# Kernel optimization log

Measured on AMD Instinct MI355X. Metric: run time of the kernel, lower is better.

Reference implementation:

```python
import jax, jax.numpy as jnp
import numpy as np

D_MODEL = 512

def setup_inputs() -> dict:
    key = jax.random.key(0)
    k1, k2, k3, k4, k5 = jax.random.split(key, 5)
    x = jax.random.normal(k1, (8, D_MODEL, 2048), dtype=jnp.float32)
    s = 1.0 / np.sqrt(D_MODEL)
    W_qkv = jax.random.uniform(k2, (D_MODEL, 3 * D_MODEL), dtype=jnp.float32, minval=-s, maxval=s)
    b_qkv = jax.random.uniform(k3, (3 * D_MODEL,), dtype=jnp.float32, minval=-s, maxval=s)
    W_proj = jax.random.uniform(k4, (D_MODEL, D_MODEL), dtype=jnp.float32, minval=-s, maxval=s)
    b_proj = jax.random.uniform(k5, (D_MODEL,), dtype=jnp.float32, minval=-s, maxval=s)
    return {"x": x, "W_qkv": W_qkv, "b_qkv": b_qkv, "W_proj": W_proj, "b_proj": b_proj}

def reference(x, W_qkv, b_qkv, W_proj, b_proj):
    # x: [B, L, N] with L == d_model; attend across the N variable axis
    xt = jnp.swapaxes(x, 1, 2)                      # [B, N, L]
    L = xt.shape[-1]
    qkv = xt @ W_qkv + b_qkv                        # [B, N, 3L]
    q, k, v = jnp.split(qkv, 3, axis=-1)            # each [B, N, L]
    attn = jnp.einsum('bnd,bmd->bnm', q, k) / jnp.sqrt(jnp.float32(L))
    attn = jax.nn.softmax(attn, axis=-1)            # [B, N, N]
    out = jnp.einsum('bnm,bmd->bnd', attn, v)       # [B, N, L]
    out = out @ W_proj + b_proj                     # [B, N, L]
    return jnp.swapaxes(out, 1, 2)                  # [B, L, N]
```

## Files before the change

### kernel.cpp

```cpp
#include <hip/hip_runtime.h>

#define NVAR 2048
#define DM   512
#define J3   1536

typedef _Float16 f16;
typedef _Float16 f16x8 __attribute__((ext_vector_type(8)));
typedef _Float16 f16x4 __attribute__((ext_vector_type(4)));
typedef float    f32x4 __attribute__((ext_vector_type(4)));

#define SBAR() do { asm volatile("s_barrier" ::: "memory"); \
                    __builtin_amdgcn_sched_barrier(0); } while(0)
#define LGKM0() do { asm volatile("s_waitcnt lgkmcnt(0)" ::: "memory"); \
                     __builtin_amdgcn_sched_barrier(0); } while(0)
#define GLOAD(gp, lp) __builtin_amdgcn_global_load_lds( \
    (const __attribute__((address_space(1))) void*)(gp), \
    (__attribute__((address_space(3))) void*)(lp), 16, 0, 0)

__device__ __forceinline__ void waitvm_n(int n) {
    switch (n) {
    case 0: asm volatile("s_waitcnt vmcnt(0)" ::: "memory"); break;
    case 1: asm volatile("s_waitcnt vmcnt(1)" ::: "memory"); break;
    case 2: asm volatile("s_waitcnt vmcnt(2)" ::: "memory"); break;
    case 3: asm volatile("s_waitcnt vmcnt(3)" ::: "memory"); break;
    case 4: asm volatile("s_waitcnt vmcnt(4)" ::: "memory"); break;
    case 5: asm volatile("s_waitcnt vmcnt(5)" ::: "memory"); break;
    case 6: asm volatile("s_waitcnt vmcnt(6)" ::: "memory"); break;
    case 7: asm volatile("s_waitcnt vmcnt(7)" ::: "memory"); break;
    case 8: asm volatile("s_waitcnt vmcnt(8)" ::: "memory"); break;
    default: break;
    }
    __builtin_amdgcn_sched_barrier(0);
}

__global__ __launch_bounds__(256)
void k_tr(const float* __restrict__ src, f16* __restrict__ dst,
          int R, int C, long bsSrc, long bsDst) {
    __shared__ float t[64][65];
    const float* s = src + (size_t)blockIdx.z * bsSrc;
    f16* d = dst + (size_t)blockIdx.z * bsDst;
    const int c0 = blockIdx.x * 64, r0 = blockIdx.y * 64;
    const int lx = threadIdx.x & 15, ly = threadIdx.x >> 4;
#pragma unroll
    for (int p = 0; p < 4; ++p) {
        int r = p * 16 + ly;
        f32x4 v = *(const f32x4*)(s + (size_t)(r0 + r) * C + c0 + lx * 4);
#pragma unroll
        for (int i = 0; i < 4; ++i) t[r][lx * 4 + i] = v[i];
    }
    __syncthreads();
#pragma unroll
    for (int p = 0; p < 4; ++p) {
        int c = p * 16 + ly;
        f16x4 h;
#pragma unroll
        for (int i = 0; i < 4; ++i) h[i] = (f16)t[lx * 4 + i][c];
        *(f16x4*)(d + (size_t)(c0 + c) * R + r0 + lx * 4) = h;
    }
}

__global__ __launch_bounds__(256)
void k_cast(const float* __restrict__ W, f16* __restrict__ out) {
    int idx = blockIdx.x * 256 + threadIdx.x;
    int gi = idx * 4;
    int d = gi >> 9, j = gi & 511;
    f32x4 v = *(const f32x4*)(W + (size_t)d * J3 + 1024 + j);
    f16x4 h;
#pragma unroll
    for (int i = 0; i < 4; ++i) h[i] = (f16)v[i];
    *(f16x4*)(out + (size_t)d * 512 + j) = h;
}

__global__ __launch_bounds__(256)
void k_bvp(const float* __restrict__ bqkv, const float* __restrict__ Wp,
           float* __restrict__ bias_c) {
    const int b = blockIdx.x;
    const int lt = threadIdx.x & 63, js = threadIdx.x >> 6;
    const int l = b * 64 + lt;
    float s = 0.f;
    for (int j = js * 128; j < js * 128 + 128; ++j)
        s += bqkv[1024 + j] * Wp[(size_t)j * DM + l];
    __shared__ float red[4][64];
    red[js][lt] = s;
    __syncthreads();
    if (js == 0)
        bias_c[1024 + l] = (red[0][lt] + red[1][lt]) + (red[2][lt] + red[3][lt]);
    if (threadIdx.x < 128) {
        int i = b * 128 + threadIdx.x;
        bias_c[i] = bqkv[i];
    }
}

#define ASZ (256 * 64)
__global__ __launch_bounds__(512, 2)
void gemm_sp(const f16* __restrict__ A, const f16* __restrict__ B,
             long bsA, long bsB, int lda, int ldb, int K,
             float scale, f16* __restrict__ o0) {
    __shared__ f16 smem[5 * ASZ];
    f16* sA = smem;
    f16* sB = smem + 3 * ASZ;

    const int tid  = threadIdx.x;
    const int lane = tid & 63;
    const int w    = __builtin_amdgcn_readfirstlane(tid >> 6);
    const int wm   = (w >> 2) * 128;
    const int wn   = (w & 3) * 64;
    const int z    = blockIdx.x;
    const int bid  = blockIdx.y;
    const int bxA  = bid & 7;
    const int bxB  = bid >> 3;

    const f16* Ab = A + (size_t)z * bsA + (size_t)bxA * 256 * lda;
    const f16* Bb = B + (size_t)z * bsB + (size_t)bxB * 256 * ldb;

    int offA[2][2], offB[2][2];
#pragma unroll
    for (int h = 0; h < 2; ++h)
#pragma unroll
        for (int i = 0; i < 2; ++i) {
            int slot = i * 512 + tid;
            int row  = h * 128 + (slot >> 3);
            int s    = (slot & 7) ^ (row & 7);
            offA[h][i] = row * lda + s * 8;
            offB[h][i] = row * ldb + s * 8;
        }

    auto STG_A = [&](int kt, int h, int buf) {
        f16* d = sA + buf * ASZ + h * 8192;
#pragma unroll
        for (int i = 0; i < 2; ++i)
            GLOAD(Ab + offA[h][i] + kt * 64, d + (i * 512 + tid) * 8);
    };
    auto STG_B = [&](int kt, int h, int buf) {
        f16* d = sB + buf * ASZ + h * 8192;
#pragma unroll
        for (int i = 0; i < 2; ++i)
            GLOAD(Bb + offB[h][i] + kt * 64, d + (i * 512 + tid) * 8);
    };

    int koff[2];
#pragma unroll
    for (int ks = 0; ks < 2; ++ks)
        koff[ks] = ((ks * 4 + (lane >> 4)) ^ (lane & 7)) * 8;
    const int rowA = (wm + (lane & 15)) * 64;
    const int rowB = (wn + (lane & 15)) * 64;

    f16x8 av[8][2], bv[4][2];
    f32x4 acc[8][4] = {};

    auto LD_AV = [&](const f16* p, int mi0) {
#pragma unroll
        for (int mi = 0; mi < 4; ++mi)
#pragma unroll
            for (int ks = 0; ks < 2; ++ks)
                av[mi0 + mi][ks] = *(const f16x8*)(p + rowA + (mi0 + mi) * 1024 + koff[ks]);
    };
    auto LD_BV = [&](const f16* p, int nj0) {
#pragma unroll
        for (int nj = 0; nj < 2; ++nj)
#pragma unroll
            for (int ks = 0; ks < 2; ++ks)
                bv[nj0 + nj][ks] = *(const f16x8*)(p + rowB + (nj0 + nj) * 1024 + koff[ks]);
    };
    auto MM = [&](int mi0, int nj0) {
        __builtin_amdgcn_s_setprio(1);
#pragma unroll
        for (int mi = 0; mi < 4; ++mi)
#pragma unroll
            for (int nj = 0; nj < 2; ++nj)
#pragma unroll
                for (int ks = 0; ks < 2; ++ks)
                    acc[mi0 + mi][nj0 + nj] = __builtin_amdgcn_mfma_f32_16x16x32_f16(
                        av[mi0 + mi][ks], bv[nj0 + nj][ks], acc[mi0 + mi][nj0 + nj], 0, 0, 0);
        __builtin_amdgcn_s_setprio(0);
    };

    const int NT = K >> 6;
    int issued = 0, markB = 0;

    STG_A(0, 0, 0); STG_A(0, 1, 0); issued += 4;
    STG_B(0, 0, 0); STG_B(0, 1, 0); issued += 4; markB = issued;
    if (NT > 1) { STG_A(1, 0, 1); STG_A(1, 1, 1); issued += 4; }
    waitvm_n(issued - markB);
    SBAR();

    int iA = 0, iB = 0;
    for (int t = 0; t < NT; ++t) {
        const f16* pA = sA + iA * ASZ;
        const f16* pB = sB + iB * ASZ;
        const int bufB2 = iB ^ 1;
        int bufA2 = iA + 2; if (bufA2 >= 3) bufA2 -= 3;

        LD_BV(pB, 0); LD_AV(pA, 0);
        if (t + 1 < NT) { STG_B(t + 1, 0, bufB2); issued += 2; }
        SBAR(); LGKM0();
        MM(0, 0);
        SBAR();

        LD_BV(pB, 2);
        if (t + 1 < NT) { STG_B(t + 1, 1, bufB2); issued += 2; markB = issued; }
        SBAR(); LGKM0();
        MM(0, 2);
        SBAR();

        LD_AV(pA, 4);
        if (t + 2 < NT) { STG_A(t + 2, 0, bufA2); issued += 2; }
        SBAR(); LGKM0();
        MM(4, 2);
        SBAR();

        if (t + 2 < NT) { STG_A(t + 2, 1, bufA2); issued += 2; }
        if (t + 1 < NT) { waitvm_n(issued - markB); SBAR(); }
        MM(4, 0);
        if (t + 1 < NT) SBAR();

        iA = (iA + 1 == 3) ? 0 : iA + 1;
        iB ^= 1;
    }

    const int n0 = bxB * 256;
    const int m0 = bxA * 256;
    f16* bb = smem;
#pragma unroll
    for (int mi = 0; mi < 8; ++mi) {
        const int m    = wm + mi * 16 + ((lane >> 4) << 2);
        const int c16  = m >> 3;
        const int half = m & 4;
#pragma unroll
        for (int nj = 0; nj < 4; ++nj) {
            const int nl = wn + nj * 16 + (lane & 15);
            f16x4 vv;
#pragma unroll
            for (int r = 0; r < 4; ++r)
                vv[r] = (f16)__expf(acc[mi][nj][r] * scale);
            *(f16x4*)(bb + nl * 256 + ((c16 ^ (nl & 7)) << 3) + half) = vv;
        }
    }
    LGKM0();
    SBAR();
#pragma unroll
    for (int it = 0; it < 16; ++it) {
        const int row = it * 16 + (tid >> 5);
        const int ch  = tid & 31;
        f16x8 v = *(const f16x8*)(bb + row * 256 + ((ch ^ (row & 7)) << 3));
        *(f16x8*)(o0 + ((size_t)z * NVAR + n0 + row) * NVAR + m0 + ch * 8) = v;
    }
}

#define AO (128 * 64)
#define BO (256 * 64)
__global__ __launch_bounds__(512, 2)
void gemm_out(const f16* __restrict__ A, const f16* __restrict__ B,
              long bsA, long bsB, int lda, int ldb, int K,
              const float* __restrict__ bias, float* __restrict__ of) {
    __shared__ f16 smem[3 * AO + 2 * BO];
    f16* sA = smem;
    f16* sB = smem + 3 * AO;

    const int tid  = threadIdx.x;
    const int lane = tid & 63;
    const int w    = __builtin_amdgcn_readfirstlane(tid >> 6);
    const int wm   = (w >> 2) * 64;
    const int wn   = (w & 3) * 64;
    const int z    = blockIdx.x;
    const int bid  = blockIdx.y;
    const int bxA  = bid & 15;
    const int bxB  = bid >> 4;

    const f16* Ab = A + (size_t)z * bsA + (size_t)bxA * 128 * lda;
    const f16* Bb = B + (size_t)z * bsB + (size_t)bxB * 256 * ldb;

    int offA[2], offB[4];
#pragma unroll
    for (int i = 0; i < 2; ++i) {
        int slot = i * 512 + tid;
        int row  = slot >> 3;
        int s    = (slot & 7) ^ (row & 7);
        offA[i] = row * lda + s * 8;
    }
#pragma unroll
    for (int i = 0; i < 4; ++i) {
        int slot = i * 512 + tid;
        int row  = slot >> 3;
        int s    = (slot & 7) ^ (row & 7);
        offB[i] = row * ldb + s * 8;
    }

    auto STG_A = [&](int kt, int buf) {
        f16* d = sA + buf * AO;
#pragma unroll
        for (int i = 0; i < 2; ++i)
            GLOAD(Ab + offA[i] + kt * 64, d + (i * 512 + tid) * 8);
    };
    auto STG_B = [&](int kt, int buf) {
        f16* d = sB + buf * BO;
#pragma unroll
        for (int i = 0; i < 4; ++i)
            GLOAD(Bb + offB[i] + kt * 64, d + (i * 512 + tid) * 8);
    };

    int koff[2];
#pragma unroll
    for (int ks = 0; ks < 2; ++ks)
        koff[ks] = ((ks * 4 + (lane >> 4)) ^ (lane & 7)) * 8;
    const int rowA = (wm + (lane & 15)) * 64;
    const int rowB = (wn + (lane & 15)) * 64;

    f16x8 ones;
#pragma unroll
    for (int e = 0; e < 8; ++e) ones[e] = (f16)1.0f;

    f16x8 av[4][2], bv[4][2];
    f32x4 acc[4][4] = {};
    f32x4 accrs[4] = {};

    auto LD_AV = [&](const f16* p, int mi0) {
#pragma unroll
        for (int mi = 0; mi < 2; ++mi)
#pragma unroll
            for (int ks = 0; ks < 2; ++ks)
                av[mi0 + mi][ks] = *(const f16x8*)(p + rowA + (mi0 + mi) * 1024 + koff[ks]);
    };
    auto LD_BV = [&](const f16* p) {
#pragma unroll
        for (int nj = 0; nj < 4; ++nj)
#pragma unroll
            for (int ks = 0; ks < 2; ++ks)
                bv[nj][ks] = *(const f16x8*)(p + rowB + nj * 1024 + koff[ks]);
    };
    auto MM = [&](int mi0) {
        __builtin_amdgcn_s_setprio(1);
#pragma unroll
        for (int mi = 0; mi < 2; ++mi)
#pragma unroll
            for (int ks = 0; ks < 2; ++ks) {
                accrs[mi0 + mi] = __builtin_amdgcn_mfma_f32_16x16x32_f16(
                    av[mi0 + mi][ks], ones, accrs[mi0 + mi], 0, 0, 0);
#pragma unroll
                for (int nj = 0; nj < 4; ++nj)
                    acc[mi0 + mi][nj] = __builtin_amdgcn_mfma_f32_16x16x32_f16(
                        av[mi0 + mi][ks], bv[nj][ks], acc[mi0 + mi][nj], 0, 0, 0);
            }
        __builtin_amdgcn_s_setprio(0);
    };

    const int NT = K >> 6;
    int issued = 0, markB = 0;

    STG_A(0, 0); issued += 2;
    STG_B(0, 0); issued += 4; markB = issued;
    if (NT > 1) { STG_A(1, 1); issued += 2; }
    waitvm_n(issued - markB);
    SBAR();

    int iA = 0, iB = 0;
    for (int t = 0; t < NT; ++t) {
        const f16* pA = sA + iA * AO;
        const f16* pB = sB + iB * BO;
        int bufA2 = iA + 2; if (bufA2 >= 3) bufA2 -= 3;

        LD_BV(pB); LD_AV(pA, 0);
        if (t + 1 < NT) { STG_B(t + 1, iB ^ 1); issued += 4; markB = issued; }
        SBAR(); LGKM0();
        MM(0);
        SBAR();

        LD_AV(pA, 2);
        if (t + 2 < NT) { STG_A(t + 2, bufA2); issued += 2; }
        SBAR(); LGKM0();
        MM(2);
        if (t + 1 < NT) { waitvm_n(issued - markB); SBAR(); }

        iA = (iA + 1 == 3) ? 0 : iA + 1;
        iB ^= 1;
    }

    const int rb0 = bxA * 128 + wm + (lane >> 4) * 4;
    const int cb0 = bxB * 256 + wn + (lane & 15);
#pragma unroll
    for (int mi = 0; mi < 4; ++mi) {
        f32x4 inv;
#pragma unroll
        for (int r = 0; r < 4; ++r) inv[r] = 1.0f / accrs[mi][r];
#pragma unroll
        for (int nj = 0; nj < 4; ++nj) {
            const int l = cb0 + nj * 16;
            const float bb = bias[l];
            f32x4 vv;
#pragma unroll
            for (int r = 0; r < 4; ++r) vv[r] = acc[mi][nj][r] * inv[r] + bb;
            *(f32x4*)(of + ((size_t)z * DM + l) * NVAR + rb0 + mi * 16) = vv;
        }
    }
}

template<int MODE>
__global__ __launch_bounds__(256)
void gemm_f16(const f16* __restrict__ A, const f16* __restrict__ B,
              long bsA, long bsB, int lda, int ldb, int K, int nbx,
              const float* __restrict__ bias,
              f16* __restrict__ o0, f16* __restrict__ o1, f16* __restrict__ o2) {
    __shared__ f16 sA[128 * 64];
    __shared__ f16 sB[128 * 64];
    const int tid  = threadIdx.x;
    const int lane = tid & 63;
    const int w    = __builtin_amdgcn_readfirstlane(tid >> 6);
    const int wm   = (w >> 1) * 64;
    const int wn   = (w & 1) * 64;
    const int z    = blockIdx.x;
    const int bid  = blockIdx.y;
    const int bxA  = bid % nbx;
    const int bxB  = bid / nbx;

    const f16* Ab = A + (size_t)z * bsA + (size_t)bxA * 128 * lda;
    const f16* Bb = B + (size_t)z * bsB + (size_t)bxB * 128 * ldb;

    int srcA[4], srcB[4];
#pragma unroll
    for (int i = 0; i < 4; ++i) {
        int slot = i * 256 + tid;
        int row  = slot >> 3;
        int s    = (slot & 7) ^ (row & 7);
        srcA[i] = row * lda + s * 8;
        srcB[i] = row * ldb + s * 8;
    }

    f32x4 acc[4][4] = {};

    for (int k0 = 0; k0 < K; k0 += 64) {
        __syncthreads();
#pragma unroll
        for (int i = 0; i < 4; ++i) {
            GLOAD(Ab + srcA[i] + k0, sA + i * 2048 + w * 512);
            GLOAD(Bb + srcB[i] + k0, sB + i * 2048 + w * 512);
        }
        __syncthreads();
#pragma unroll
        for (int kh = 0; kh < 2; ++kh) {
            f16x8 av[4], bv[4];
#pragma unroll
            for (int mi = 0; mi < 4; ++mi) {
                int r = wm + mi * 16 + (lane & 15);
                int s = (kh * 4 + (lane >> 4)) ^ (r & 7);
                av[mi] = *(const f16x8*)(sA + r * 64 + s * 8);
            }
#pragma unroll
            for (int nj = 0; nj < 4; ++nj) {
                int r = wn + nj * 16 + (lane & 15);
                int s = (kh * 4 + (lane >> 4)) ^ (r & 7);
                bv[nj] = *(const f16x8*)(sB + r * 64 + s * 8);
            }
#pragma unroll
            for (int mi = 0; mi < 4; ++mi)
#pragma unroll
                for (int nj = 0; nj < 4; ++nj)
                    acc[mi][nj] = __builtin_amdgcn_mfma_f32_16x16x32_f16(
                        av[mi], bv[nj], acc[mi][nj], 0, 0, 0);
        }
    }

    const int rb0 = bxA * 128 + wm + (lane >> 4) * 4;
    const int cb0 = bxB * 128 + wn + (lane & 15);

    if (MODE == 0) {
        const int seg = (bxA * 128) >> 9;
#pragma unroll
        for (int mi = 0; mi < 4; ++mi) {
            const int j = rb0 + mi * 16;
            const f32x4 b4 = *(const f32x4*)(bias + j);
#pragma unroll
            for (int nj = 0; nj < 4; ++nj) {
                const int n = cb0 + nj * 16;
                if (seg == 2) {
#pragma unroll
                    for (int r = 0; r < 4; ++r)
                        o2[((size_t)z * DM + (j - 1024 + r)) * NVAR + n] =
                            (f16)(acc[mi][nj][r] + b4[r]);
                } else {
                    f16* dst = seg ? o1 : o0;
                    const int jj = seg ? j - 512 : j;
                    f16x4 vv;
#pragma unroll
                    for (int r = 0; r < 4; ++r) vv[r] = (f16)(acc[mi][nj][r] + b4[r]);
                    *(f16x4*)(dst + ((size_t)z * NVAR + n) * DM + jj) = vv;
                }
            }
        }
    } else {
#pragma unroll
        for (int mi = 0; mi < 4; ++mi)
#pragma unroll
            for (int nj = 0; nj < 4; ++nj) {
                f16x4 vv;
#pragma unroll
                for (int r = 0; r < 4; ++r) vv[r] = (f16)acc[mi][nj][r];
                *(f16x4*)(o0 + ((size_t)(cb0 + nj * 16)) * DM
                               + rb0 + mi * 16) = vv;
            }
    }
}

extern "C" void kernel_launch(void* const* d_in, const int* in_sizes, int n_in,
                              void* d_out, int out_size, void* d_ws, size_t ws_size,
                              hipStream_t stream) {
    const float* x     = (const float*)d_in[0];
    const float* Wqkv  = (const float*)d_in[1];
    const float* bqkv  = (const float*)d_in[2];
    const float* Wproj = (const float*)d_in[3];
    const float* bproj = (const float*)d_in[4];
    float* out = (float*)d_out;

    const size_t PB = (size_t)NVAR * DM;
    f16* xT   = (f16*)d_ws;
    f16* q    = xT + 8 * PB;
    f16* kk   = q  + 8 * PB;
    f16* vwT  = kk + 8 * PB;
    f16* S    = vwT + 8 * PB;
    f16* scr  = S  + (size_t)8 * NVAR * NVAR;
    f16* WqT  = scr + 8 * PB;
    f16* WpT  = WqT + (size_t)J3 * DM;
    f16* Wq2  = scr;
    float* bias_c = (float*)(scr + 512 * 512);

    k_tr<<<dim3(NVAR / 64, DM / 64, 8), 256, 0, stream>>>(
        x, xT, DM, NVAR, (long)DM * NVAR, (long)NVAR * DM);
    k_tr<<<dim3(16, DM / 64, 1), 256, 0, stream>>>(Wqkv, WqT, DM, J3, 0, 0);
    k_tr<<<dim3(DM / 64, DM / 64, 1), 256, 0, stream>>>(Wproj, WpT, DM, DM, 0, 0);
    k_cast<<<dim3(256), 256, 0, stream>>>(Wqkv, Wq2);
    k_bvp<<<dim3(8), 256, 0, stream>>>(bqkv, Wproj, bias_c);

    gemm_f16<4><<<dim3(1, 16), 256, 0, stream>>>(
        Wq2, WpT, 0, 0, 512, DM, DM, 4,
        nullptr, WqT + (size_t)1024 * DM, nullptr, nullptr);

    gemm_f16<0><<<dim3(8, 12 * 16), 256, 0, stream>>>(
        WqT, xT, 0, (long)NVAR * DM, DM, DM, DM, 12,
        bias_c, q, kk, vwT);

    gemm_sp<<<dim3(8, 8 * 8), 512, 0, stream>>>(
        kk, q, (long)NVAR * DM, (long)NVAR * DM, DM, DM, DM,
        0.044194173824159216f, S);

    gemm_out<<<dim3(8, 32), 512, 0, stream>>>(
        S, vwT, (long)NVAR * NVAR, (long)DM * NVAR, NVAR, NVAR, NVAR,
        bproj, out);
}
```

Measured before the change: 173.6 us.

## Split QKV projection into large-tile QK GEMM and separate V GEMM

```diff
diff --git a/kernel.cpp b/kernel.cpp
--- a/kernel.cpp
+++ b/kernel.cpp
@@ -60,42 +60,69 @@
 }
 
 __global__ __launch_bounds__(256)
-void k_cast(const float* __restrict__ W, f16* __restrict__ out) {
-    int idx = blockIdx.x * 256 + threadIdx.x;
-    int gi = idx * 4;
-    int d = gi >> 9, j = gi & 511;
-    f32x4 v = *(const f32x4*)(W + (size_t)d * J3 + 1024 + j);
-    f16x4 h;
-#pragma unroll
-    for (int i = 0; i < 4; ++i) h[i] = (f16)v[i];
-    *(f16x4*)(out + (size_t)d * 512 + j) = h;
-}
-
-__global__ __launch_bounds__(256)
-void k_bvp(const float* __restrict__ bqkv, const float* __restrict__ Wp,
-           float* __restrict__ bias_c) {
+void k_prep(const float* __restrict__ Wqkv, const float* __restrict__ Wproj,
+            const float* __restrict__ bqkv,
+            f16* __restrict__ WqT, f16* __restrict__ WpT,
+            f16* __restrict__ Wq2, float* __restrict__ bias_c) {
+    __shared__ float t[64][65];
     const int b = blockIdx.x;
-    const int lt = threadIdx.x & 63, js = threadIdx.x >> 6;
-    const int l = b * 64 + lt;
-    float s = 0.f;
-    for (int j = js * 128; j < js * 128 + 128; ++j)
-        s += bqkv[1024 + j] * Wp[(size_t)j * DM + l];
-    __shared__ float red[4][64];
-    red[js][lt] = s;
-    __syncthreads();
-    if (js == 0)
-        bias_c[1024 + l] = (red[0][lt] + red[1][lt]) + (red[2][lt] + red[3][lt]);
-    if (threadIdx.x < 128) {
-        int i = b * 128 + threadIdx.x;
-        bias_c[i] = bqkv[i];
+    if (b < 192) {
+        const float* s; f16* d; int R, C, bx, by;
+        if (b < 128) { s = Wqkv; d = WqT; R = DM; C = J3; bx = b & 15; by = b >> 4; }
+        else { s = Wproj; d = WpT; R = DM; C = DM; bx = (b - 128) & 7; by = (b - 128) >> 3; }
+        const int c0 = bx * 64, r0 = by * 64;
+        const int lx = threadIdx.x & 15, ly = threadIdx.x >> 4;
+#pragma unroll
+        for (int p = 0; p < 4; ++p) {
+            int r = p * 16 + ly;
+            f32x4 v = *(const f32x4*)(s + (size_t)(r0 + r) * C + c0 + lx * 4);
+#pragma unroll
+            for (int i = 0; i < 4; ++i) t[r][lx * 4 + i] = v[i];
+        }
+        __syncthreads();
+#pragma unroll
+        for (int p = 0; p < 4; ++p) {
+            int c = p * 16 + ly;
+            f16x4 h;
+#pragma unroll
+            for (int i = 0; i < 4; ++i) h[i] = (f16)t[lx * 4 + i][c];
+            *(f16x4*)(d + (size_t)(c0 + c) * R + r0 + lx * 4) = h;
+        }
+    } else if (b < 448) {
+        int idx = (b - 192) * 256 + threadIdx.x;
+        int gi = idx * 4;
+        int d = gi >> 9, j = gi & 511;
+        f32x4 v = *(const f32x4*)(Wqkv + (size_t)d * J3 + 1024 + j);
+        f16x4 h;
+#pragma unroll
+        for (int i = 0; i < 4; ++i) h[i] = (f16)v[i];
+        *(f16x4*)(Wq2 + (size_t)d * 512 + j) = h;
+    } else {
+        const int bb = b - 448;
+        const int lt = threadIdx.x & 63, js = threadIdx.x >> 6;
+        const int l = bb * 64 + lt;
+        float s = 0.f;
+        for (int j = js * 128; j < js * 128 + 128; ++j)
+            s += bqkv[1024 + j] * Wproj[(size_t)j * DM + l];
+        float* red = &t[0][0];
+        red[js * 64 + lt] = s;
+        __syncthreads();
+        if (js == 0)
+            bias_c[1024 + l] = (red[lt] + red[64 + lt]) + (red[128 + lt] + red[192 + lt]);
+        if (threadIdx.x < 128) {
+            int i = bb * 128 + threadIdx.x;
+            bias_c[i] = bqkv[i];
+        }
     }
 }
 
 #define ASZ (256 * 64)
+template<int MODE, int ABITS>
 __global__ __launch_bounds__(512, 2)
 void gemm_sp(const f16* __restrict__ A, const f16* __restrict__ B,
              long bsA, long bsB, int lda, int ldb, int K,
-             float scale, f16* __restrict__ o0) {
+             const float* __restrict__ bias, float scale,
+             f16* __restrict__ o0, f16* __restrict__ o1) {
     __shared__ f16 smem[5 * ASZ];
     f16* sA = smem;
     f16* sB = smem + 3 * ASZ;
@@ -107,8 +134,8 @@
     const int wn   = (w & 3) * 64;
     const int z    = blockIdx.x;
     const int bid  = blockIdx.y;
-    const int bxA  = bid & 7;
-    const int bxB  = bid >> 3;
+    const int bxA  = bid & ((1 << ABITS) - 1);
+    const int bxB  = bid >> ABITS;
 
     const f16* Ab = A + (size_t)z * bsA + (size_t)bxA * 256 * lda;
     const f16* Bb = B + (size_t)z * bsB + (size_t)bxB * 256 * ldb;
@@ -218,32 +245,53 @@
         iB ^= 1;
     }
 
-    const int n0 = bxB * 256;
-    const int m0 = bxA * 256;
-    f16* bb = smem;
-#pragma unroll
-    for (int mi = 0; mi < 8; ++mi) {
-        const int m    = wm + mi * 16 + ((lane >> 4) << 2);
-        const int c16  = m >> 3;
-        const int half = m & 4;
-#pragma unroll
-        for (int nj = 0; nj < 4; ++nj) {
-            const int nl = wn + nj * 16 + (lane & 15);
-            f16x4 vv;
-#pragma unroll
-            for (int r = 0; r < 4; ++r)
-                vv[r] = (f16)__expf(acc[mi][nj][r] * scale);
-            *(f16x4*)(bb + nl * 256 + ((c16 ^ (nl & 7)) << 3) + half) = vv;
-        }
-    }
-    LGKM0();
-    SBAR();
-#pragma unroll
-    for (int it = 0; it < 16; ++it) {
-        const int row = it * 16 + (tid >> 5);
-        const int ch  = tid & 31;
-        f16x8 v = *(const f16x8*)(bb + row * 256 + ((ch ^ (row & 7)) << 3));
-        *(f16x8*)(o0 + ((size_t)z * NVAR + n0 + row) * NVAR + m0 + ch * 8) = v;
+    if (MODE == 0) {
+        const int seg = bxA >> 1;
+        f16* dst = seg ? o1 : o0;
+        const int rb0 = bxA * 256 + wm + (lane >> 4) * 4;
+        const int cb0 = bxB * 256 + wn + (lane & 15);
+#pragma unroll
+        for (int mi = 0; mi < 8; ++mi) {
+            const int j = rb0 + mi * 16;
+            const int jj = j - seg * 512;
+            const f32x4 b4 = *(const f32x4*)(bias + j);
+#pragma unroll
+            for (int nj = 0; nj < 4; ++nj) {
+                const int n = cb0 + nj * 16;
+                f16x4 vv;
+#pragma unroll
+                for (int r = 0; r < 4; ++r) vv[r] = (f16)(acc[mi][nj][r] + b4[r]);
+                *(f16x4*)(dst + ((size_t)z * NVAR + n) * DM + jj) = vv;
+            }
+        }
+    } else {
+        const int n0 = bxB * 256;
+        const int m0 = bxA * 256;
+        f16* bb = smem;
+#pragma unroll
+        for (int mi = 0; mi < 8; ++mi) {
+            const int m    = wm + mi * 16 + ((lane >> 4) << 2);
+            const int c16  = m >> 3;
+            const int half = m & 4;
+#pragma unroll
+            for (int nj = 0; nj < 4; ++nj) {
+                const int nl = wn + nj * 16 + (lane & 15);
+                f16x4 vv;
+#pragma unroll
+                for (int r = 0; r < 4; ++r)
+                    vv[r] = (f16)__expf(acc[mi][nj][r] * scale);
+                *(f16x4*)(bb + nl * 256 + ((c16 ^ (nl & 7)) << 3) + half) = vv;
+            }
+        }
+        LGKM0();
+        SBAR();
+#pragma unroll
+        for (int it = 0; it < 16; ++it) {
+            const int row = it * 16 + (tid >> 5);
+            const int ch  = tid & 31;
+            f16x8 v = *(const f16x8*)(bb + row * 256 + ((ch ^ (row & 7)) << 3));
+            *(f16x8*)(o0 + ((size_t)z * NVAR + n0 + row) * NVAR + m0 + ch * 8) = v;
+        }
     }
 }
 
@@ -398,8 +446,7 @@
 __global__ __launch_bounds__(256)
 void gemm_f16(const f16* __restrict__ A, const f16* __restrict__ B,
               long bsA, long bsB, int lda, int ldb, int K, int nbx,
-              const float* __restrict__ bias,
-              f16* __restrict__ o0, f16* __restrict__ o1, f16* __restrict__ o2) {
+              const float* __restrict__ bias, f16* __restrict__ o0) {
     __shared__ f16 sA[128 * 64];
     __shared__ f16 sB[128 * 64];
     const int tid  = threadIdx.x;
@@ -462,31 +509,7 @@
     const int rb0 = bxA * 128 + wm + (lane >> 4) * 4;
     const int cb0 = bxB * 128 + wn + (lane & 15);
 
-    if (MODE == 0) {
-        const int seg = (bxA * 128) >> 9;
-#pragma unroll
-        for (int mi = 0; mi < 4; ++mi) {
-            const int j = rb0 + mi * 16;
-            const f32x4 b4 = *(const f32x4*)(bias + j);
-#pragma unroll
-            for (int nj = 0; nj < 4; ++nj) {
-                const int n = cb0 + nj * 16;
-                if (seg == 2) {
-#pragma unroll
-                    for (int r = 0; r < 4; ++r)
-                        o2[((size_t)z * DM + (j - 1024 + r)) * NVAR + n] =
-                            (f16)(acc[mi][nj][r] + b4[r]);
-                } else {
-                    f16* dst = seg ? o1 : o0;
-                    const int jj = seg ? j - 512 : j;
-                    f16x4 vv;
-#pragma unroll
-                    for (int r = 0; r < 4; ++r) vv[r] = (f16)(acc[mi][nj][r] + b4[r]);
-                    *(f16x4*)(dst + ((size_t)z * NVAR + n) * DM + jj) = vv;
-                }
-            }
-        }
-    } else {
+    if (MODE == 4) {
 #pragma unroll
         for (int mi = 0; mi < 4; ++mi)
 #pragma unroll
@@ -496,6 +519,18 @@
                 for (int r = 0; r < 4; ++r) vv[r] = (f16)acc[mi][nj][r];
                 *(f16x4*)(o0 + ((size_t)(cb0 + nj * 16)) * DM
                                + rb0 + mi * 16) = vv;
+            }
+    } else {
+#pragma unroll
+        for (int mi = 0; mi < 4; ++mi)
+#pragma unroll
+            for (int nj = 0; nj < 4; ++nj) {
+                const int l = cb0 + nj * 16;
+                const float bb = bias[l];
+                f16x4 vv;
+#pragma unroll
+                for (int r = 0; r < 4; ++r) vv[r] = (f16)(acc[mi][nj][r] + bb);
+                *(f16x4*)(o0 + ((size_t)z * DM + l) * NVAR + rb0 + mi * 16) = vv;
             }
     }
 }
@@ -518,28 +553,29 @@
     f16* S    = vwT + 8 * PB;
     f16* scr  = S  + (size_t)8 * NVAR * NVAR;
     f16* WqT  = scr + 8 * PB;
+    f16* WvpT = WqT + (size_t)1024 * DM;
     f16* WpT  = WqT + (size_t)J3 * DM;
     f16* Wq2  = scr;
     float* bias_c = (float*)(scr + 512 * 512);
 
     k_tr<<<dim3(NVAR / 64, DM / 64, 8), 256, 0, stream>>>(
         x, xT, DM, NVAR, (long)DM * NVAR, (long)NVAR * DM);
-    k_tr<<<dim3(16, DM / 64, 1), 256, 0, stream>>>(Wqkv, WqT, DM, J3, 0, 0);
-    k_tr<<<dim3(DM / 64, DM / 64, 1), 256, 0, stream>>>(Wproj, WpT, DM, DM, 0, 0);
-    k_cast<<<dim3(256), 256, 0, stream>>>(Wqkv, Wq2);
-    k_bvp<<<dim3(8), 256, 0, stream>>>(bqkv, Wproj, bias_c);
+    k_prep<<<dim3(456), 256, 0, stream>>>(Wqkv, Wproj, bqkv, WqT, WpT, Wq2, bias_c);
 
     gemm_f16<4><<<dim3(1, 16), 256, 0, stream>>>(
-        Wq2, WpT, 0, 0, 512, DM, DM, 4,
-        nullptr, WqT + (size_t)1024 * DM, nullptr, nullptr);
-
-    gemm_f16<0><<<dim3(8, 12 * 16), 256, 0, stream>>>(
-        WqT, xT, 0, (long)NVAR * DM, DM, DM, DM, 12,
-        bias_c, q, kk, vwT);
-
-    gemm_sp<<<dim3(8, 8 * 8), 512, 0, stream>>>(
+        Wq2, WpT, 0, 0, 512, DM, DM, 4, nullptr, WvpT);
+
+    gemm_sp<0, 2><<<dim3(8, 4 * 8), 512, 0, stream>>>(
+        WqT, xT, 0, (long)NVAR * DM, DM, DM, DM,
+        bias_c, 1.f, q, kk);
+
+    gemm_f16<5><<<dim3(8, 16 * 4), 256, 0, stream>>>(
+        xT, WvpT, (long)NVAR * DM, 0, DM, DM, DM, 16,
+        bias_c + 1024, vwT);
+
+    gemm_sp<1, 3><<<dim3(8, 8 * 8), 512, 0, stream>>>(
         kk, q, (long)NVAR * DM, (long)NVAR * DM, DM, DM, DM,
-        0.044194173824159216f, S);
+        nullptr, 0.044194173824159216f, S, nullptr);
 
     gemm_out<<<dim3(8, 32), 512, 0, stream>>>(
         S, vwT, (long)NVAR * NVAR, (long)DM * NVAR, NVAR, NVAR, NVAR,
```

Result: slower. 178.2 us (+2.6%).
